# Kernel optimization log

Measured on AMD Instinct MI355X. Metric: run time of the kernel, lower is better.

## Reference

```python
import jax, jax.numpy as jnp
import numpy as np

TAU_MEM = 0.005   # sinabs LIF tau_mem (in time-step units)
THR = 1.0         # default spike_threshold
BATCH = 16        # LIFSqueeze batch_size; leading dim is BATCH * T
BETA = 10.0       # surrogate gradient sharpness (sinabs SingleExponential default)


@jax.custom_vjp
def spike_fn(v):
    # MultiSpike: number of spikes = floor(v / thr), clipped at 0
    return jnp.floor(jnp.clip(v / THR, 0.0, None))

def _spike_fwd(v):
    return spike_fn(v), v

def _spike_bwd(v, g):
    # single-exponential surrogate gradient around threshold
    return (g * jnp.exp(-BETA * jnp.abs(v - THR)),)

spike_fn.defvjp(_spike_fwd, _spike_bwd)


def lif(x, spiking=True):
    """LIFSqueeze: x is (BATCH*T, ...); unfold time, scan LIF dynamics, refold."""
    alpha = jnp.exp(jnp.asarray(-1.0 / TAU_MEM, x.dtype))
    T = x.shape[0] // BATCH
    xt = jnp.swapaxes(x.reshape(BATCH, T, *x.shape[1:]), 0, 1)  # (T, B, ...)

    def step(v, xin):
        v = alpha * v + (1.0 - alpha) * xin  # norm_input=True: decay + scaled input
        if spiking:
            s = spike_fn(v)
            return v - s * THR, s            # membrane-subtract reset
        return v, v                          # spike_fn=None -> leaky integrator readout

    _, out = jax.lax.scan(step, jnp.zeros_like(xt[0]), xt)
    return jnp.swapaxes(out, 0, 1).reshape(x.shape)


def conv(x, w, stride, pad):
    return jax.lax.conv_general_dilated(
        x, w, (stride, stride), [(pad, pad), (pad, pad)],
        dimension_numbers=("NCHW", "OIHW", "NCHW"))


def maxpool2(x):
    return jax.lax.reduce_window(x, -jnp.inf, jax.lax.max,
                                 (1, 1, 2, 2), (1, 1, 2, 2), "VALID")


def setup_inputs() -> dict:
    key = jax.random.key(0)
    k = jax.random.split(key, 5)
    x = jax.random.normal(k[0], (1024, 2, 128, 128), jnp.float32)  # (B*T, C, H, W)
    w1 = jax.random.normal(k[1], (8, 2, 2, 2), jnp.float32) * (1.0 / np.sqrt(2 * 4))
    w2 = jax.random.normal(k[2], (8, 8, 3, 3), jnp.float32) * (1.0 / np.sqrt(8 * 9))
    w3 = jax.random.normal(k[3], (8, 8, 3, 3), jnp.float32) * (1.0 / np.sqrt(8 * 9))
    w_fc = jax.random.normal(k[4], (2, 512), jnp.float32) * (1.0 / np.sqrt(512))
    return {"x": x, "w1": w1, "w2": w2, "w3": w3, "w_fc": w_fc}


def reference(x, w1, w2, w3, w_fc):
    h = lif(conv(x, w1, 2, 0))        # (N, 8, 64, 64)
    h = maxpool2(h)                   # (N, 8, 32, 32)
    h = lif(conv(h, w2, 1, 1))
    h = maxpool2(h)                   # (N, 8, 16, 16)
    h = lif(conv(h, w3, 1, 1))
    h = maxpool2(h)                   # (N, 8, 8, 8)
    h = h.reshape(h.shape[0], -1)     # (N, 512)
    h = h @ w_fc.T                    # (N, 2)
    return lif(h, spiking=False)      # membrane-potential readout
```

## Files before the change

kernel.cpp:

```cpp
#include <hip/hip_runtime.h>
#include <cstddef>


__global__ __launch_bounds__(256, 4) void fused_snn(
    const float* __restrict__ x,
    const float* __restrict__ w1,
    const float* __restrict__ w2,
    const float* __restrict__ w3,
    const float* __restrict__ wfc,
    float* __restrict__ out)
{
    __shared__ __align__(16) float t1[8][34][34];
    __shared__ __align__(16) float t2[8][18][18];
    __shared__ float red[8];

    const int n = blockIdx.x;
    const int t = threadIdx.x;

    for (int i = t; i < 8 * 34 * 34; i += 256) (&t1[0][0][0])[i] = 0.f;
    for (int i = t; i < 8 * 18 * 18; i += 256) (&t2[0][0][0])[i] = 0.f;

    float wa[64];
#pragma unroll
    for (int i = 0; i < 64; ++i) wa[i] = w1[i];
    __syncthreads();

    {
        const float* xb = x + (size_t)n * (2 * 128 * 128);
#pragma unroll 1
        for (int k = 0; k < 4; ++k) {
            int i = (k << 8) + t;
            int py = i >> 5, px = i & 31;
            float p[2][4][4];
#pragma unroll
            for (int c = 0; c < 2; ++c)
#pragma unroll
                for (int r = 0; r < 4; ++r) {
                    float4 v = *reinterpret_cast<const float4*>(
                        xb + (c * 128 + 4 * py + r) * 128 + 4 * px);
                    p[c][r][0] = v.x; p[c][r][1] = v.y; p[c][r][2] = v.z; p[c][r][3] = v.w;
                }
#pragma unroll
            for (int co = 0; co < 8; ++co) {
                float m = 0.f;
#pragma unroll
                for (int oy = 0; oy < 2; ++oy)
#pragma unroll
                for (int ox = 0; ox < 2; ++ox) {
                    float a = 0.f;
#pragma unroll
                    for (int c = 0; c < 2; ++c)
#pragma unroll
                    for (int kh = 0; kh < 2; ++kh)
#pragma unroll
                    for (int kw = 0; kw < 2; ++kw)
                        a += p[c][2 * oy + kh][2 * ox + kw] * wa[((co * 2 + c) * 2 + kh) * 2 + kw];
                    m = fmaxf(m, floorf(fmaxf(a, 0.f)));
                }
                t1[co][py + 1][px + 1] = m;
            }
        }
    }
    __syncthreads();

    {
        const int py = t >> 4, px = t & 15;
        float acc[8][2][2];
#pragma unroll
        for (int i = 0; i < 32; ++i) (&acc[0][0][0])[i] = 0.f;

#pragma unroll 1
        for (int ci = 0; ci < 8; ++ci) {
            float p[4][4];
#pragma unroll
            for (int r = 0; r < 4; ++r) {
                const float2* row = reinterpret_cast<const float2*>(&t1[ci][2 * py + r][0]);
                float2 a = row[px], b = row[px + 1];
                p[r][0] = a.x; p[r][1] = a.y; p[r][2] = b.x; p[r][3] = b.y;
            }
#pragma unroll
            for (int co = 0; co < 8; ++co) {
                const float* wp = w2 + (co * 8 + ci) * 9;
                float wv[9];
#pragma unroll
                for (int i = 0; i < 9; ++i) wv[i] = wp[i];
#pragma unroll
                for (int oy = 0; oy < 2; ++oy)
#pragma unroll
                for (int ox = 0; ox < 2; ++ox) {
                    float a = acc[co][oy][ox];
#pragma unroll
                    for (int kh = 0; kh < 3; ++kh)
#pragma unroll
                    for (int kw = 0; kw < 3; ++kw)
                        a += p[oy + kh][ox + kw] * wv[kh * 3 + kw];
                    acc[co][oy][ox] = a;
                }
            }
        }
#pragma unroll
        for (int co = 0; co < 8; ++co) {
            float m = 0.f;
#pragma unroll
            for (int oy = 0; oy < 2; ++oy)
#pragma unroll
            for (int ox = 0; ox < 2; ++ox)
                m = fmaxf(m, floorf(fmaxf(acc[co][oy][ox], 0.f)));
            t2[co][py + 1][px + 1] = m;
        }
    }
    __syncthreads();

    {
        const int co2 = __builtin_amdgcn_readfirstlane(t >> 6);
        const int l = t & 63;
        const int py = l >> 3, px = l & 7;

        float acc[2][2][2];
#pragma unroll
        for (int i = 0; i < 8; ++i) (&acc[0][0][0])[i] = 0.f;

#pragma unroll 1
        for (int ci = 0; ci < 8; ++ci) {
            float p[4][4];
#pragma unroll
            for (int r = 0; r < 4; ++r) {
                const float2* row = reinterpret_cast<const float2*>(&t2[ci][2 * py + r][0]);
                float2 a = row[px], b = row[px + 1];
                p[r][0] = a.x; p[r][1] = a.y; p[r][2] = b.x; p[r][3] = b.y;
            }
#pragma unroll
            for (int cc = 0; cc < 2; ++cc) {
                const float* wp = w3 + ((2 * co2 + cc) * 8 + ci) * 9;
                float wv[9];
#pragma unroll
                for (int i = 0; i < 9; ++i) wv[i] = wp[i];
#pragma unroll
                for (int oy = 0; oy < 2; ++oy)
#pragma unroll
                for (int ox = 0; ox < 2; ++ox) {
                    float a = acc[cc][oy][ox];
#pragma unroll
                    for (int kh = 0; kh < 3; ++kh)
#pragma unroll
                    for (int kw = 0; kw < 3; ++kw)
                        a += p[oy + kh][ox + kw] * wv[kh * 3 + kw];
                    acc[cc][oy][ox] = a;
                }
            }
        }

        float p0 = 0.f, p1 = 0.f;
#pragma unroll
        for (int cc = 0; cc < 2; ++cc) {
            float m = 0.f;
#pragma unroll
            for (int oy = 0; oy < 2; ++oy)
#pragma unroll
            for (int ox = 0; ox < 2; ++ox)
                m = fmaxf(m, floorf(fmaxf(acc[cc][oy][ox], 0.f)));
            int o = (2 * co2 + cc) * 64 + l;
            p0 += m * wfc[o];
            p1 += m * wfc[512 + o];
        }

#pragma unroll
        for (int off = 32; off > 0; off >>= 1) {
            p0 += __shfl_down(p0, off);
            p1 += __shfl_down(p1, off);
        }
        if (l == 0) { red[co2 * 2 + 0] = p0; red[co2 * 2 + 1] = p1; }
    }
    __syncthreads();

    if (t == 0) {
        out[n * 2 + 0] = red[0] + red[2] + red[4] + red[6];
        out[n * 2 + 1] = red[1] + red[3] + red[5] + red[7];
    }
}

extern "C" void kernel_launch(void* const* d_in, const int* in_sizes, int n_in,
                              void* d_out, int out_size, void* d_ws, size_t ws_size,
                              hipStream_t stream) {
    const float* x   = (const float*)d_in[0];
    const float* w1  = (const float*)d_in[1];
    const float* w2  = (const float*)d_in[2];
    const float* w3  = (const float*)d_in[3];
    const float* wfc = (const float*)d_in[4];
    float* outp = (float*)d_out;

    fused_snn<<<1024, 256, 0, stream>>>(x, w1, w2, w3, wfc, outp);
}
```

Baseline: 209.8 us.

## Store first pooled feature map as bf16 in LDS and raise occupancy target

The first shared tile now holds bf16 values instead of fp32, which halves its LDS footprint. The launch-bounds occupancy hint rises from 4 to 5 blocks per CU to use that room. Stage 1 also loads input rows in two halves and keeps a running max per channel, which lowers register pressure. The stored values are floored non-negative spike counts, so bf16 is exact only while they stay small. The extra unpack shifts in the conv2 read path add some ALU work.

```diff
diff --git a/kernel.cpp b/kernel.cpp
--- a/kernel.cpp
+++ b/kernel.cpp
@@ -2,7 +2,17 @@
 #include <cstddef>
 
 
-__global__ __launch_bounds__(256, 4) void fused_snn(
+__device__ __forceinline__ float bf_lo(unsigned int u) {
+    union { unsigned int i; float f; } c; c.i = u << 16; return c.f;
+}
+__device__ __forceinline__ float bf_hi(unsigned int u) {
+    union { unsigned int i; float f; } c; c.i = u & 0xffff0000u; return c.f;
+}
+__device__ __forceinline__ unsigned short f2bf(float f) {
+    union { float f; unsigned int i; } c; c.f = f; return (unsigned short)(c.i >> 16);
+}
+
+__global__ __launch_bounds__(256, 5) void fused_snn(
     const float* __restrict__ x,
     const float* __restrict__ w1,
     const float* __restrict__ w2,
@@ -10,15 +20,18 @@
     const float* __restrict__ wfc,
     float* __restrict__ out)
 {
-    __shared__ __align__(16) float t1[8][34][34];
+    __shared__ unsigned short t1[8][34][34];
     __shared__ __align__(16) float t2[8][18][18];
     __shared__ float red[8];
 
     const int n = blockIdx.x;
     const int t = threadIdx.x;
 
-    for (int i = t; i < 8 * 34 * 34; i += 256) (&t1[0][0][0])[i] = 0.f;
-    for (int i = t; i < 8 * 18 * 18; i += 256) (&t2[0][0][0])[i] = 0.f;
+    {
+        unsigned int* z1 = (unsigned int*)&t1[0][0][0];
+        for (int i = t; i < 4624; i += 256) z1[i] = 0u;
+        for (int i = t; i < 8 * 18 * 18; i += 256) (&t2[0][0][0])[i] = 0.f;
+    }
 
     float wa[64];
 #pragma unroll
@@ -31,34 +44,40 @@
         for (int k = 0; k < 4; ++k) {
             int i = (k << 8) + t;
             int py = i >> 5, px = i & 31;
-            float p[2][4][4];
-#pragma unroll
-            for (int c = 0; c < 2; ++c)
-#pragma unroll
-                for (int r = 0; r < 4; ++r) {
-                    float4 v = *reinterpret_cast<const float4*>(
-                        xb + (c * 128 + 4 * py + r) * 128 + 4 * px);
-                    p[c][r][0] = v.x; p[c][r][1] = v.y; p[c][r][2] = v.z; p[c][r][3] = v.w;
+
+            float res[8];
+#pragma unroll
+            for (int co = 0; co < 8; ++co) res[co] = 0.f;
+
+#pragma unroll
+            for (int half = 0; half < 2; ++half) {
+                float p[2][2][4];
+#pragma unroll
+                for (int c = 0; c < 2; ++c)
+#pragma unroll
+                    for (int r = 0; r < 2; ++r) {
+                        float4 v = *reinterpret_cast<const float4*>(
+                            xb + (c * 128 + 4 * py + 2 * half + r) * 128 + 4 * px);
+                        p[c][r][0] = v.x; p[c][r][1] = v.y; p[c][r][2] = v.z; p[c][r][3] = v.w;
+                    }
+#pragma unroll
+                for (int ox = 0; ox < 2; ++ox)
+#pragma unroll
+                for (int co = 0; co < 8; ++co) {
+                    float a = 0.f;
+#pragma unroll
+                    for (int c = 0; c < 2; ++c)
+#pragma unroll
+                    for (int kh = 0; kh < 2; ++kh)
+#pragma unroll
+                    for (int kw = 0; kw < 2; ++kw)
+                        a += p[c][kh][2 * ox + kw] * wa[((co * 2 + c) * 2 + kh) * 2 + kw];
+                    res[co] = fmaxf(res[co], floorf(fmaxf(a, 0.f)));
                 }
-#pragma unroll
-            for (int co = 0; co < 8; ++co) {
-                float m = 0.f;
-#pragma unroll
-                for (int oy = 0; oy < 2; ++oy)
-#pragma unroll
-                for (int ox = 0; ox < 2; ++ox) {
-                    float a = 0.f;
-#pragma unroll
-                    for (int c = 0; c < 2; ++c)
-#pragma unroll
-                    for (int kh = 0; kh < 2; ++kh)
-#pragma unroll
-                    for (int kw = 0; kw < 2; ++kw)
-                        a += p[c][2 * oy + kh][2 * ox + kw] * wa[((co * 2 + c) * 2 + kh) * 2 + kw];
-                    m = fmaxf(m, floorf(fmaxf(a, 0.f)));
-                }
-                t1[co][py + 1][px + 1] = m;
-            }
+            }
+#pragma unroll
+            for (int co = 0; co < 8; ++co)
+                t1[co][py + 1][px + 1] = f2bf(res[co]);
         }
     }
     __syncthreads();
@@ -74,9 +93,11 @@
             float p[4][4];
 #pragma unroll
             for (int r = 0; r < 4; ++r) {
-                const float2* row = reinterpret_cast<const float2*>(&t1[ci][2 * py + r][0]);
-                float2 a = row[px], b = row[px + 1];
-                p[r][0] = a.x; p[r][1] = a.y; p[r][2] = b.x; p[r][3] = b.y;
+                const unsigned int* rp = (const unsigned int*)&t1[ci][2 * py + r][0];
+                unsigned int u0 = rp[px];
+                unsigned int u1 = rp[px + 1];
+                p[r][0] = bf_lo(u0); p[r][1] = bf_hi(u0);
+                p[r][2] = bf_lo(u1); p[r][3] = bf_hi(u1);
             }
 #pragma unroll
             for (int co = 0; co < 8; ++co) {
```

Result: slower. 214.6 us (+2.3%).
